# Kernel tuning notes

Measured on AMD Instinct MI355X. Metric: run time of the kernel, lower is better.

The kernel has to match this reference:

```python
import jax, jax.numpy as jnp
import numpy as np

N = 500_000
LEVELS = 3
GDIM = 8
BASE_H = 128
BASE_W = 128
COND = 64
DOUT = 128
HID = 2
DIN = 1 + 2 * LEVELS * GDIM  # rho + theta-grid feats + rho-grid feats = 49


def _bilinear(grid, u, v):
    # grid: [H, W, D]; u, v in [0,1]; u indexes W axis, v indexes H axis.
    H, W, D = grid.shape
    x = u * (W - 1)
    y = v * (H - 1)
    x0 = jnp.clip(jnp.floor(x).astype(jnp.int32), 0, W - 2)
    y0 = jnp.clip(jnp.floor(y).astype(jnp.int32), 0, H - 2)
    x1 = x0 + 1
    y1 = y0 + 1
    wx = (x - x0)[:, None]
    wy = (y - y0)[:, None]
    g = grid.reshape(H * W, D)
    c00 = jnp.take(g, y0 * W + x0, axis=0)
    c01 = jnp.take(g, y0 * W + x1, axis=0)
    c10 = jnp.take(g, y1 * W + x0, axis=0)
    c11 = jnp.take(g, y1 * W + x1, axis=0)
    return (c00 * (1 - wx) * (1 - wy) + c01 * wx * (1 - wy)
            + c10 * (1 - wx) * wy + c11 * wx * wy)


def setup_inputs() -> dict:
    key = jax.random.key(0)
    ks = jax.random.split(key, 24)
    inp = {
        'coords': jax.random.uniform(ks[0], (N,), dtype=jnp.float32),
        'angles': jax.random.uniform(ks[1], (N,), dtype=jnp.float32),
        'rho': jax.random.normal(ks[2], (N,), dtype=jnp.float32),
        'rho_n': jax.random.uniform(ks[3], (N,), dtype=jnp.float32),
        'curve_feats': jax.random.normal(ks[4], (N, COND), dtype=jnp.float32),
        'type_sample': jax.random.normal(ks[5], (N, DOUT), dtype=jnp.float32),
    }
    # Multi-resolution grids (theta-conditioned and rho-conditioned).
    for l in range(LEVELS):
        h, w = BASE_H * 2 ** l, BASE_W * 2 ** l
        inp[f'gt{l}'] = 0.1 * jax.random.normal(ks[6 + l], (h, w, GDIM), dtype=jnp.float32)
        inp[f'gr{l}'] = 0.1 * jax.random.normal(ks[9 + l], (h, w, GDIM), dtype=jnp.float32)
    # FiLM-modulated encoder chain (block 0 + HID residual blocks).
    inp['film0_fcW'] = jax.random.normal(ks[12], (DIN, DOUT), dtype=jnp.float32) / np.sqrt(DIN)
    inp['film0_fcb'] = jnp.zeros((DOUT,), dtype=jnp.float32)
    inp['filmh_fcW'] = jax.random.normal(ks[13], (HID, DOUT, DOUT), dtype=jnp.float32) / np.sqrt(DOUT)
    inp['filmh_fcb'] = jnp.zeros((HID, DOUT), dtype=jnp.float32)
    inp['gammaW'] = 0.02 * jax.random.normal(ks[14], (HID + 1, COND, DOUT), dtype=jnp.float32)
    inp['gammab'] = jnp.ones((HID + 1, DOUT), dtype=jnp.float32)
    inp['betaW'] = 0.02 * jax.random.normal(ks[15], (HID + 1, COND, DOUT), dtype=jnp.float32)
    inp['betab'] = jnp.zeros((HID + 1, DOUT), dtype=jnp.float32)
    # Decoder MLP [DOUT, 64, 1].
    inp['decW1'] = jax.random.normal(ks[16], (DOUT, 64), dtype=jnp.float32) / np.sqrt(DOUT)
    inp['decb1'] = jnp.zeros((64,), dtype=jnp.float32)
    inp['decW2'] = jax.random.normal(ks[17], (64, 1), dtype=jnp.float32) / 8.0
    inp['decb2'] = jnp.zeros((1,), dtype=jnp.float32)
    return inp


def reference(coords, angles, rho, rho_n, curve_feats, type_sample,
              gt0, gt1, gt2, gr0, gr1, gr2,
              film0_fcW, film0_fcb, filmh_fcW, filmh_fcb,
              gammaW, gammab, betaW, betab,
              decW1, decb1, decW2, decb2):
    # Multi-res grid interpolation, concat across levels.
    ct = jnp.concatenate([_bilinear(g, angles, coords) for g in (gt0, gt1, gt2)], axis=-1)
    cr = jnp.concatenate([_bilinear(g, rho_n, coords) for g in (gr0, gr1, gr2)], axis=-1)
    feat = jnp.concatenate([rho[:, None], ct, cr], axis=-1)  # [N, DIN]
    # FiLM conditioning: gamma/beta per block from curve_feats.
    gamma = jnp.einsum('nc,lcd->lnd', curve_feats, gammaW) + gammab[:, None, :]
    beta = jnp.einsum('nc,lcd->lnd', curve_feats, betaW) + betab[:, None, :]
    # Block 0 + type_sample residual.
    x = jax.nn.silu(gamma[0] * (feat @ film0_fcW + film0_fcb) + beta[0]) + type_sample
    # Residual FiLM blocks.
    for i in range(filmh_fcW.shape[0]):
        x = x + jax.nn.silu(gamma[i + 1] * (x @ filmh_fcW[i] + filmh_fcb[i]) + beta[i + 1])
    # Decoder MLP.
    h = jax.nn.relu(x @ decW1 + decb1)
    sdf = (h @ decW2 + decb2)[..., 0]  # [N]
    return sdf
```

## Files before the change

### kernel.cpp

```cpp
#include <hip/hip_runtime.h>
#include <stdint.h>

typedef short s16x8 __attribute__((ext_vector_type(8)));
typedef float f32x4 __attribute__((ext_vector_type(4)));
typedef uint32_t u32x4 __attribute__((ext_vector_type(4)));

#define MFMA16(a, b, c) __builtin_amdgcn_mfma_f32_16x16x32_bf16(a, b, c, 0, 0, 0)

__device__ __forceinline__ short f2bf(float f) {
  uint32_t u = __builtin_bit_cast(uint32_t, f);
  u += 0x7FFFu + ((u >> 16) & 1u);
  return (short)(u >> 16);
}
__device__ __forceinline__ uint32_t cvtpk(float lo, float hi) {
  uint32_t r;
  asm("v_cvt_pk_bf16_f32 %0, %1, %2" : "=v"(r) : "v"(lo), "v"(hi));
  return r;
}
__device__ __forceinline__ short f2bf1(float f) { return (short)cvtpk(f, f); }

__global__ void pack_w(const float* __restrict__ w0, const float* __restrict__ wh,
                       const float* __restrict__ gw, const float* __restrict__ bw,
                       const float* __restrict__ d1, const float* __restrict__ d1bp,
                       const float* __restrict__ d2wp, short* __restrict__ out,
                       float* __restrict__ dpk) {
  int idx = blockIdx.x * 512 + threadIdx.x;
  if (idx < 98304) {
    int f = idx >> 9;
    int r = idx & 511;
    int lane = r >> 3, e = r & 7;
    int kk = ((lane >> 4) << 3) + e;
    int nn = lane & 15;
    float v;
    if (f < 16) {
      int ct = f >> 1, ks = f & 1;
      int k = ks * 32 + kk, n = ct * 16 + nn;
      if (k < 48) v = w0[(1 + k) * 128 + n];
      else if (k == 48) v = w0[n];
      else v = 0.f;
    } else if (f < 112) {
      int f2 = f - 16;
      int ks = f2 & 1, ct = (f2 >> 1) & 7, gb = (f2 >> 4) & 1, l = f2 >> 5;
      int k = ks * 32 + kk, n = ct * 16 + nn;
      const float* Wp = gb ? bw : gw;
      v = Wp[(l * 64 + k) * 128 + n];
    } else if (f < 176) {
      int f2 = f - 112;
      int ks = f2 & 3, ct = (f2 >> 2) & 7, i = f2 >> 5;
      int k = ks * 32 + kk, n = ct * 16 + nn;
      v = wh[(i * 128 + k) * 128 + n];
    } else {
      int f2 = f - 176;
      int ks = f2 & 3, ct = f2 >> 2;
      int k = ks * 32 + kk, n = ct * 16 + nn;
      v = d1[k * 64 + n];
    }
    out[idx] = f2bf(v);
  } else if (idx < 100352) {
    int j = idx - 98304;
    int which = j >> 10;
    int k = j & 1023;
    int ct = k >> 8, lane = (k >> 2) & 63, rr = k & 3;
    int n2 = ct * 16 + ((lane >> 4) << 2) + rr;
    dpk[j] = which ? d2wp[n2] : d1bp[n2];
  }
}

__global__ __launch_bounds__(512) void ngc_gather(
    const float* __restrict__ coords, const float* __restrict__ angles,
    const float* __restrict__ rho, const float* __restrict__ rho_n,
    const float* __restrict__ gt0, const float* __restrict__ gr0,
    const float* __restrict__ gt1, const float* __restrict__ gr1,
    const float* __restrict__ gt2, const float* __restrict__ gr2,
    short* __restrict__ stage, int n, int t0) {
  const int tid = threadIdx.x;
  const int row0 = (t0 + blockIdx.x) * 64;
  char* st = (char*)(stage + (size_t)blockIdx.x * 4096);

  if (tid < 384) {
    int r = tid & 63, g = tid >> 6;
    int gr_ = row0 + r; gr_ = gr_ < n ? gr_ : n - 1;
    float vv = coords[gr_];
    float u = (g < 3) ? angles[gr_] : rho_n[gr_];
    int lvl = (g < 3) ? g : g - 3;
    const float* G = (g == 0) ? gt0 : (g == 1) ? gt1 : (g == 2) ? gt2
                   : (g == 3) ? gr0 : (g == 4) ? gr1 : gr2;
    int Wg = 128 << lvl;
    float x = u * (float)(Wg - 1), y = vv * (float)(Wg - 1);
    int ix = (int)x; ix = ix < 0 ? 0 : (ix > Wg - 2 ? Wg - 2 : ix);
    int iy = (int)y; iy = iy < 0 ? 0 : (iy > Wg - 2 ? Wg - 2 : iy);
    float wx = x - (float)ix, wy = y - (float)iy;
    const float4* p0 = (const float4*)(G + (size_t)(iy * Wg + ix) * 8);
    const float4* p1 = (const float4*)(G + (size_t)((iy + 1) * Wg + ix) * 8);
    float4 c00a = p0[0], c00b = p0[1], c01a = p0[2], c01b = p0[3];
    float4 c10a = p1[0], c10b = p1[1], c11a = p1[2], c11b = p1[3];
    float w00 = (1.f - wx) * (1.f - wy), w01 = wx * (1.f - wy);
    float w10 = (1.f - wx) * wy, w11 = wx * wy;
    float e0 = c00a.x * w00 + c01a.x * w01 + c10a.x * w10 + c11a.x * w11;
    float e1 = c00a.y * w00 + c01a.y * w01 + c10a.y * w10 + c11a.y * w11;
    float e2 = c00a.z * w00 + c01a.z * w01 + c10a.z * w10 + c11a.z * w11;
    float e3 = c00a.w * w00 + c01a.w * w01 + c10a.w * w10 + c11a.w * w11;
    float e4 = c00b.x * w00 + c01b.x * w01 + c10b.x * w10 + c11b.x * w11;
    float e5 = c00b.y * w00 + c01b.y * w01 + c10b.y * w10 + c11b.y * w11;
    float e6 = c00b.z * w00 + c01b.z * w01 + c10b.z * w10 + c11b.z * w11;
    float e7 = c00b.w * w00 + c01b.w * w01 + c10b.w * w10 + c11b.w * w11;
    u32x4 o = { cvtpk(e0, e1), cvtpk(e2, e3), cvtpk(e4, e5), cvtpk(e6, e7) };
    int dst16 = ((r >> 4) * 2 + (g >> 2)) * 64 + (g & 3) * 16 + (r & 15);
    *(u32x4*)(st + dst16 * 16) = o;
  } else if (tid < 448) {
    int r = tid - 384;
    int gr_ = row0 + r; gr_ = gr_ < n ? gr_ : n - 1;
    s16x8 a = { f2bf1(rho[gr_]), 0, 0, 0, 0, 0, 0, 0 };
    int base = ((r >> 4) * 2 + 1) * 64;
    *(s16x8*)(st + (base + 32 + (r & 15)) * 16) = a;
  } else {
    int r = tid - 448;
    s16x8 z = { 0, 0, 0, 0, 0, 0, 0, 0 };
    int base = ((r >> 4) * 2 + 1) * 64;
    *(s16x8*)(st + (base + 48 + (r & 15)) * 16) = z;
  }
}

__global__ __launch_bounds__(512) void ngc_gemm(
    const float* __restrict__ cf, const float* __restrict__ ts,
    const float* __restrict__ f0b, const float* __restrict__ fhb,
    const float* __restrict__ gab, const float* __restrict__ beb,
    const float* __restrict__ d2b, const short* __restrict__ pw,
    const float* __restrict__ dpk, const short* __restrict__ stage,
    float* __restrict__ out, int n, int t0) {
  __shared__ __align__(16) char smem[40 * 1024];
  char* cfA = smem;
  char* x0  = smem + 8 * 1024;
  char* x1  = smem + 24 * 1024;

  const int tid = threadIdx.x;
  const int lane = tid & 63;
  const int w = tid >> 6;
  const int g16 = lane >> 4;
  const int l15 = lane & 15;
  const int row0 = (t0 + blockIdx.x) * 64;
  const int col = w * 16 + l15;
  const int cbase = col >> 5;
  const int cslot = ((col >> 3) & 3) * 16;
  const int ce = (col & 7) * 2;

  const float d2b0 = d2b[0];

  float tsr[4][4];
#pragma unroll
  for (int rg = 0; rg < 4; ++rg)
#pragma unroll
    for (int rr = 0; rr < 4; ++rr) {
      int grow = row0 + rg * 16 + g16 * 4 + rr; grow = grow < n ? grow : n - 1;
      tsr[rg][rr] = ts[(size_t)grow * 128 + col];
    }

  {
    int cb = tid & 7, r = tid >> 3;
    int gr_ = row0 + r; gr_ = gr_ < n ? gr_ : n - 1;
    const float4* cp = (const float4*)(cf + (size_t)gr_ * 64 + cb * 8);
    float4 v0 = cp[0], v1 = cp[1];
    u32x4 s = { cvtpk(v0.x, v0.y), cvtpk(v0.z, v0.w),
                cvtpk(v1.x, v1.y), cvtpk(v1.z, v1.w) };
    int dst16 = ((r >> 4) * 2 + (cb >> 2)) * 64 + (cb & 3) * 16 + (r & 15);
    *(u32x4*)(cfA + dst16 * 16) = s;
  }
  __syncthreads();

  const s16x8* fB = (const s16x8*)stage + (size_t)blockIdx.x * 512;
  auto ldfeat = [&](int frag) -> s16x8 { return fB[frag * 64 + lane]; };
  auto ldF = [&](const char* b, int frag) -> s16x8 {
    return *(const s16x8*)(b + (frag * 64 + lane) * 16);
  };
  auto ldw = [&](int frag) -> s16x8 { return ((const s16x8*)pw)[frag * 64 + lane]; };

  float xr[4][4];

  {
    s16x8 bw0 = ldw(w * 2), bw1 = ldw(w * 2 + 1);
    s16x8 bg0 = ldw(16 + w * 2), bg1 = ldw(16 + w * 2 + 1);
    s16x8 bb0 = ldw(32 + w * 2), bb1 = ldw(32 + w * 2 + 1);
    float f0bv = f0b[col], gabv = gab[col], bebv = beb[col];
#pragma unroll
    for (int rg = 0; rg < 4; ++rg) {
      s16x8 a0 = ldfeat(rg * 2), a1 = ldfeat(rg * 2 + 1);
      s16x8 c0 = ldF(cfA, rg * 2), c1 = ldF(cfA, rg * 2 + 1);
      f32x4 t = {0.f, 0.f, 0.f, 0.f};
      t = MFMA16(a0, bw0, t); t = MFMA16(a1, bw1, t);
      f32x4 ga = {0.f, 0.f, 0.f, 0.f};
      ga = MFMA16(c0, bg0, ga); ga = MFMA16(c1, bg1, ga);
      f32x4 be = {0.f, 0.f, 0.f, 0.f};
      be = MFMA16(c0, bb0, be); be = MFMA16(c1, bb1, be);
      char* xbase = x0 + (rg * 4 + cbase) * 1024 + ce;
#pragma unroll
      for (int rr = 0; rr < 4; ++rr) {
        float z = (ga[rr] + gabv) * (t[rr] + f0bv) + (be[rr] + bebv);
        float sl = z * __builtin_amdgcn_rcpf(1.f + __expf(-z));
        xr[rg][rr] = sl + tsr[rg][rr];
        *(short*)(xbase + (cslot + g16 * 4 + rr) * 16) = f2bf1(xr[rg][rr]);
      }
    }
  }
  __syncthreads();

#pragma unroll
  for (int i = 0; i < 2; ++i) {
    const char* xsrc = i ? x1 : x0;
    char* xdst = i ? x0 : x1;
    s16x8 bh0 = ldw(112 + i * 32 + w * 4);
    s16x8 bh1 = ldw(112 + i * 32 + w * 4 + 1);
    s16x8 bh2 = ldw(112 + i * 32 + w * 4 + 2);
    s16x8 bh3 = ldw(112 + i * 32 + w * 4 + 3);
    s16x8 bg0 = ldw(16 + (i + 1) * 32 + w * 2);
    s16x8 bg1 = ldw(16 + (i + 1) * 32 + w * 2 + 1);
    s16x8 bb0 = ldw(16 + (i + 1) * 32 + 16 + w * 2);
    s16x8 bb1 = ldw(16 + (i + 1) * 32 + 16 + w * 2 + 1);
    float fhbv = fhb[i * 128 + col];
    float gabv = gab[(i + 1) * 128 + col];
    float bebv = beb[(i + 1) * 128 + col];
#pragma unroll
    for (int rg = 0; rg < 4; ++rg) {
      s16x8 xa = ldF(xsrc, rg * 4), xb = ldF(xsrc, rg * 4 + 1);
      s16x8 xc = ldF(xsrc, rg * 4 + 2), xd = ldF(xsrc, rg * 4 + 3);
      s16x8 c0 = ldF(cfA, rg * 2), c1 = ldF(cfA, rg * 2 + 1);
      f32x4 t = {0.f, 0.f, 0.f, 0.f};
      t = MFMA16(xa, bh0, t); t = MFMA16(xb, bh1, t);
      t = MFMA16(xc, bh2, t); t = MFMA16(xd, bh3, t);
      f32x4 ga = {0.f, 0.f, 0.f, 0.f};
      ga = MFMA16(c0, bg0, ga); ga = MFMA16(c1, bg1, ga);
      f32x4 be = {0.f, 0.f, 0.f, 0.f};
      be = MFMA16(c0, bb0, be); be = MFMA16(c1, bb1, be);
      char* xbase = xdst + (rg * 4 + cbase) * 1024 + ce;
#pragma unroll
      for (int rr = 0; rr < 4; ++rr) {
        float zz = (ga[rr] + gabv) * (t[rr] + fhbv) + (be[rr] + bebv);
        xr[rg][rr] += zz * __builtin_amdgcn_rcpf(1.f + __expf(-zz));
        *(short*)(xbase + (cslot + g16 * 4 + rr) * 16) = f2bf1(xr[rg][rr]);
      }
    }
    __syncthreads();
  }

  if (w < 4) {
    const int rg = w;
    s16x8 xF0 = ldF(x0, rg * 4), xF1 = ldF(x0, rg * 4 + 1);
    s16x8 xF2 = ldF(x0, rg * 4 + 2), xF3 = ldF(x0, rg * 4 + 3);
    float s = 0.f;
#pragma unroll
    for (int ct = 0; ct < 4; ++ct) {
      f32x4 hh = {0.f, 0.f, 0.f, 0.f};
      hh = MFMA16(ldw(176 + ct * 4 + 0), xF0, hh);
      hh = MFMA16(ldw(176 + ct * 4 + 1), xF1, hh);
      hh = MFMA16(ldw(176 + ct * 4 + 2), xF2, hh);
      hh = MFMA16(ldw(176 + ct * 4 + 3), xF3, hh);
      f32x4 db = *(const f32x4*)&dpk[ct * 256 + lane * 4];
      f32x4 wv = *(const f32x4*)&dpk[1024 + ct * 256 + lane * 4];
#pragma unroll
      for (int rr = 0; rr < 4; ++rr)
        s += fmaxf(hh[rr] + db[rr], 0.f) * wv[rr];
    }
    s += __shfl_xor(s, 16);
    s += __shfl_xor(s, 32);
    if (g16 == 0) {
      int grow = row0 + rg * 16 + l15;
      if (grow < n) out[grow] = s + d2b0;
    }
  }
}

extern "C" void kernel_launch(void* const* d_in, const int* in_sizes, int n_in,
                              void* d_out, int out_size, void* d_ws, size_t ws_size,
                              hipStream_t stream) {
  int n = in_sizes[0];
  short* pw = (short*)d_ws;
  float* dpk = (float*)((char*)d_ws + 192 * 1024);
  const size_t stage_off = 256 * 1024;
  short* stage = (short*)((char*)d_ws + stage_off);
  int ntiles = (n + 63) / 64;
  long long avail = (long long)ws_size - (long long)stage_off;
  int chunk = (int)(avail > 8192 ? avail / 8192 : 1);
  if (chunk > ntiles) chunk = ntiles;
  if (chunk < 1) chunk = 1;

  pack_w<<<196, 512, 0, stream>>>(
      (const float*)d_in[12],
      (const float*)d_in[14],
      (const float*)d_in[16],
      (const float*)d_in[18],
      (const float*)d_in[20],
      (const float*)d_in[21],
      (const float*)d_in[22],
      pw, dpk);

  for (int t0 = 0; t0 < ntiles; t0 += chunk) {
    int nb = ntiles - t0 < chunk ? ntiles - t0 : chunk;
    ngc_gather<<<nb, 512, 0, stream>>>(
        (const float*)d_in[0],
        (const float*)d_in[1],
        (const float*)d_in[2],
        (const float*)d_in[3],
        (const float*)d_in[6],
        (const float*)d_in[7],
        (const float*)d_in[8],
        (const float*)d_in[9],
        (const float*)d_in[10],
        (const float*)d_in[11],
        stage, n, t0);
    ngc_gemm<<<nb, 512, 0, stream>>>(
        (const float*)d_in[4],
        (const float*)d_in[5],
        (const float*)d_in[13],
        (const float*)d_in[15],
        (const float*)d_in[17],
        (const float*)d_in[19],
        (const float*)d_in[23],
        pw, dpk, stage, (float*)d_out, n, t0);
  }
}
```

Baseline: 271.5 us.

## Make GEMM kernel persistent with software-prefetch of next tile's inputs

The GEMM kernel becomes a grid-stride persistent loop capped at 1024 blocks. Each block prefetches the next tile's curve features and type_sample rows into registers while it computes the current tile. __syncthreads is replaced with a barrier that waits only on LDS (lgkmcnt), so the outstanding global prefetches are not drained at each barrier. This aims to hide global load latency and cut block launch overhead, at the cost of extra register pressure.

```diff
diff --git a/kernel.cpp b/kernel.cpp
--- a/kernel.cpp
+++ b/kernel.cpp
@@ -6,6 +6,7 @@
 typedef uint32_t u32x4 __attribute__((ext_vector_type(4)));
 
 #define MFMA16(a, b, c) __builtin_amdgcn_mfma_f32_16x16x32_bf16(a, b, c, 0, 0, 0)
+#define GEMM_BLK 1024
 
 __device__ __forceinline__ short f2bf(float f) {
   uint32_t u = __builtin_bit_cast(uint32_t, f);
@@ -18,6 +19,12 @@
   return r;
 }
 __device__ __forceinline__ short f2bf1(float f) { return (short)cvtpk(f, f); }
+
+__device__ __forceinline__ void bsync() {
+  asm volatile("s_waitcnt lgkmcnt(0)" ::: "memory");
+  __builtin_amdgcn_s_barrier();
+  asm volatile("" ::: "memory");
+}
 
 __global__ void pack_w(const float* __restrict__ w0, const float* __restrict__ wh,
                        const float* __restrict__ gw, const float* __restrict__ bw,
@@ -127,7 +134,7 @@
     const float* __restrict__ gab, const float* __restrict__ beb,
     const float* __restrict__ d2b, const short* __restrict__ pw,
     const float* __restrict__ dpk, const short* __restrict__ stage,
-    float* __restrict__ out, int n, int t0) {
+    float* __restrict__ out, int n, int t0, int ntc) {
   __shared__ __align__(16) char smem[40 * 1024];
   char* cfA = smem;
   char* x0  = smem + 8 * 1024;
@@ -138,132 +145,147 @@
   const int w = tid >> 6;
   const int g16 = lane >> 4;
   const int l15 = lane & 15;
-  const int row0 = (t0 + blockIdx.x) * 64;
   const int col = w * 16 + l15;
   const int cbase = col >> 5;
   const int cslot = ((col >> 3) & 3) * 16;
   const int ce = (col & 7) * 2;
+  const int cb = tid & 7, rcf = tid >> 3;
 
   const float d2b0 = d2b[0];
 
+  float4 cfr0, cfr1;
   float tsr[4][4];
-#pragma unroll
-  for (int rg = 0; rg < 4; ++rg)
-#pragma unroll
-    for (int rr = 0; rr < 4; ++rr) {
-      int grow = row0 + rg * 16 + g16 * 4 + rr; grow = grow < n ? grow : n - 1;
-      tsr[rg][rr] = ts[(size_t)grow * 128 + col];
-    }
-
-  {
-    int cb = tid & 7, r = tid >> 3;
-    int gr_ = row0 + r; gr_ = gr_ < n ? gr_ : n - 1;
+
+  auto issueA = [&](int tt2) {
+    int gr_ = (t0 + tt2) * 64 + rcf; gr_ = gr_ < n ? gr_ : n - 1;
     const float4* cp = (const float4*)(cf + (size_t)gr_ * 64 + cb * 8);
-    float4 v0 = cp[0], v1 = cp[1];
-    u32x4 s = { cvtpk(v0.x, v0.y), cvtpk(v0.z, v0.w),
-                cvtpk(v1.x, v1.y), cvtpk(v1.z, v1.w) };
-    int dst16 = ((r >> 4) * 2 + (cb >> 2)) * 64 + (cb & 3) * 16 + (r & 15);
-    *(u32x4*)(cfA + dst16 * 16) = s;
-  }
-  __syncthreads();
-
-  const s16x8* fB = (const s16x8*)stage + (size_t)blockIdx.x * 512;
-  auto ldfeat = [&](int frag) -> s16x8 { return fB[frag * 64 + lane]; };
+    cfr0 = cp[0]; cfr1 = cp[1];
+  };
+  auto issueT = [&](int tt2) {
+    int row0n = (t0 + tt2) * 64;
+#pragma unroll
+    for (int rg = 0; rg < 4; ++rg)
+#pragma unroll
+      for (int rr = 0; rr < 4; ++rr) {
+        int grow = row0n + rg * 16 + g16 * 4 + rr; grow = grow < n ? grow : n - 1;
+        tsr[rg][rr] = ts[(size_t)grow * 128 + col];
+      }
+  };
+
   auto ldF = [&](const char* b, int frag) -> s16x8 {
     return *(const s16x8*)(b + (frag * 64 + lane) * 16);
   };
   auto ldw = [&](int frag) -> s16x8 { return ((const s16x8*)pw)[frag * 64 + lane]; };
 
-  float xr[4][4];
-
-  {
-    s16x8 bw0 = ldw(w * 2), bw1 = ldw(w * 2 + 1);
-    s16x8 bg0 = ldw(16 + w * 2), bg1 = ldw(16 + w * 2 + 1);
-    s16x8 bb0 = ldw(32 + w * 2), bb1 = ldw(32 + w * 2 + 1);
-    float f0bv = f0b[col], gabv = gab[col], bebv = beb[col];
-#pragma unroll
-    for (int rg = 0; rg < 4; ++rg) {
-      s16x8 a0 = ldfeat(rg * 2), a1 = ldfeat(rg * 2 + 1);
-      s16x8 c0 = ldF(cfA, rg * 2), c1 = ldF(cfA, rg * 2 + 1);
-      f32x4 t = {0.f, 0.f, 0.f, 0.f};
-      t = MFMA16(a0, bw0, t); t = MFMA16(a1, bw1, t);
-      f32x4 ga = {0.f, 0.f, 0.f, 0.f};
-      ga = MFMA16(c0, bg0, ga); ga = MFMA16(c1, bg1, ga);
-      f32x4 be = {0.f, 0.f, 0.f, 0.f};
-      be = MFMA16(c0, bb0, be); be = MFMA16(c1, bb1, be);
-      char* xbase = x0 + (rg * 4 + cbase) * 1024 + ce;
-#pragma unroll
-      for (int rr = 0; rr < 4; ++rr) {
-        float z = (ga[rr] + gabv) * (t[rr] + f0bv) + (be[rr] + bebv);
-        float sl = z * __builtin_amdgcn_rcpf(1.f + __expf(-z));
-        xr[rg][rr] = sl + tsr[rg][rr];
-        *(short*)(xbase + (cslot + g16 * 4 + rr) * 16) = f2bf1(xr[rg][rr]);
-      }
-    }
-  }
-  __syncthreads();
-
-#pragma unroll
-  for (int i = 0; i < 2; ++i) {
-    const char* xsrc = i ? x1 : x0;
-    char* xdst = i ? x0 : x1;
-    s16x8 bh0 = ldw(112 + i * 32 + w * 4);
-    s16x8 bh1 = ldw(112 + i * 32 + w * 4 + 1);
-    s16x8 bh2 = ldw(112 + i * 32 + w * 4 + 2);
-    s16x8 bh3 = ldw(112 + i * 32 + w * 4 + 3);
-    s16x8 bg0 = ldw(16 + (i + 1) * 32 + w * 2);
-    s16x8 bg1 = ldw(16 + (i + 1) * 32 + w * 2 + 1);
-    s16x8 bb0 = ldw(16 + (i + 1) * 32 + 16 + w * 2);
-    s16x8 bb1 = ldw(16 + (i + 1) * 32 + 16 + w * 2 + 1);
-    float fhbv = fhb[i * 128 + col];
-    float gabv = gab[(i + 1) * 128 + col];
-    float bebv = beb[(i + 1) * 128 + col];
-#pragma unroll
-    for (int rg = 0; rg < 4; ++rg) {
-      s16x8 xa = ldF(xsrc, rg * 4), xb = ldF(xsrc, rg * 4 + 1);
-      s16x8 xc = ldF(xsrc, rg * 4 + 2), xd = ldF(xsrc, rg * 4 + 3);
-      s16x8 c0 = ldF(cfA, rg * 2), c1 = ldF(cfA, rg * 2 + 1);
-      f32x4 t = {0.f, 0.f, 0.f, 0.f};
-      t = MFMA16(xa, bh0, t); t = MFMA16(xb, bh1, t);
-      t = MFMA16(xc, bh2, t); t = MFMA16(xd, bh3, t);
-      f32x4 ga = {0.f, 0.f, 0.f, 0.f};
-      ga = MFMA16(c0, bg0, ga); ga = MFMA16(c1, bg1, ga);
-      f32x4 be = {0.f, 0.f, 0.f, 0.f};
-      be = MFMA16(c0, bb0, be); be = MFMA16(c1, bb1, be);
-      char* xbase = xdst + (rg * 4 + cbase) * 1024 + ce;
-#pragma unroll
-      for (int rr = 0; rr < 4; ++rr) {
-        float zz = (ga[rr] + gabv) * (t[rr] + fhbv) + (be[rr] + bebv);
-        xr[rg][rr] += zz * __builtin_amdgcn_rcpf(1.f + __expf(-zz));
-        *(short*)(xbase + (cslot + g16 * 4 + rr) * 16) = f2bf1(xr[rg][rr]);
-      }
-    }
-    __syncthreads();
-  }
-
-  if (w < 4) {
-    const int rg = w;
-    s16x8 xF0 = ldF(x0, rg * 4), xF1 = ldF(x0, rg * 4 + 1);
-    s16x8 xF2 = ldF(x0, rg * 4 + 2), xF3 = ldF(x0, rg * 4 + 3);
-    float s = 0.f;
-#pragma unroll
-    for (int ct = 0; ct < 4; ++ct) {
-      f32x4 hh = {0.f, 0.f, 0.f, 0.f};
-      hh = MFMA16(ldw(176 + ct * 4 + 0), xF0, hh);
-      hh = MFMA16(ldw(176 + ct * 4 + 1), xF1, hh);
-      hh = MFMA16(ldw(176 + ct * 4 + 2), xF2, hh);
-      hh = MFMA16(ldw(176 + ct * 4 + 3), xF3, hh);
-      f32x4 db = *(const f32x4*)&dpk[ct * 256 + lane * 4];
-      f32x4 wv = *(const f32x4*)&dpk[1024 + ct * 256 + lane * 4];
-#pragma unroll
-      for (int rr = 0; rr < 4; ++rr)
-        s += fmaxf(hh[rr] + db[rr], 0.f) * wv[rr];
-    }
-    s += __shfl_xor(s, 16);
-    s += __shfl_xor(s, 32);
-    if (g16 == 0) {
-      int grow = row0 + rg * 16 + l15;
-      if (grow < n) out[grow] = s + d2b0;
+  int tt = blockIdx.x;
+  if (tt < ntc) { issueA(tt); issueT(tt); }
+
+  for (; tt < ntc; tt += gridDim.x) {
+    const int row0 = (t0 + tt) * 64;
+    const int tn = tt + gridDim.x;
+    const s16x8* fB = (const s16x8*)stage + (size_t)tt * 512;
+
+    {
+      u32x4 s = { cvtpk(cfr0.x, cfr0.y), cvtpk(cfr0.z, cfr0.w),
+                  cvtpk(cfr1.x, cfr1.y), cvtpk(cfr1.z, cfr1.w) };
+      int dst16 = ((rcf >> 4) * 2 + (cb >> 2)) * 64 + (cb & 3) * 16 + (rcf & 15);
+      *(u32x4*)(cfA + dst16 * 16) = s;
+    }
+    if (tn < ntc) issueA(tn);
+    bsync();
+
+    float xr[4][4];
+
+    {
+      s16x8 bw0 = ldw(w * 2), bw1 = ldw(w * 2 + 1);
+      s16x8 bg0 = ldw(16 + w * 2), bg1 = ldw(16 + w * 2 + 1);
+      s16x8 bb0 = ldw(32 + w * 2), bb1 = ldw(32 + w * 2 + 1);
+      float f0bv = f0b[col], gabv = gab[col], bebv = beb[col];
+#pragma unroll
+      for (int rg = 0; rg < 4; ++rg) {
+        s16x8 a0 = fB[(rg * 2) * 64 + lane], a1 = fB[(rg * 2 + 1) * 64 + lane];
+        s16x8 c0 = ldF(cfA, rg * 2), c1 = ldF(cfA, rg * 2 + 1);
+        f32x4 t = {0.f, 0.f, 0.f, 0.f};
+        t = MFMA16(a0, bw0, t); t = MFMA16(a1, bw1, t);
+        f32x4 ga = {0.f, 0.f, 0.f, 0.f};
+        ga = MFMA16(c0, bg0, ga); ga = MFMA16(c1, bg1, ga);
+        f32x4 be = {0.f, 0.f, 0.f, 0.f};
+        be = MFMA16(c0, bb0, be); be = MFMA16(c1, bb1, be);
+        char* xbase = x0 + (rg * 4 + cbase) * 1024 + ce;
+#pragma unroll
+        for (int rr = 0; rr < 4; ++rr) {
+          float z = (ga[rr] + gabv) * (t[rr] + f0bv) + (be[rr] + bebv);
+          float sl = z * __builtin_amdgcn_rcpf(1.f + __expf(-z));
+          xr[rg][rr] = sl + tsr[rg][rr];
+          *(short*)(xbase + (cslot + g16 * 4 + rr) * 16) = f2bf1(xr[rg][rr]);
+        }
+      }
+    }
+    if (tn < ntc) issueT(tn);
+    bsync();
+
+#pragma unroll
+    for (int i = 0; i < 2; ++i) {
+      const char* xsrc = i ? x1 : x0;
+      char* xdst = i ? x0 : x1;
+      s16x8 bh0 = ldw(112 + i * 32 + w * 4);
+      s16x8 bh1 = ldw(112 + i * 32 + w * 4 + 1);
+      s16x8 bh2 = ldw(112 + i * 32 + w * 4 + 2);
+      s16x8 bh3 = ldw(112 + i * 32 + w * 4 + 3);
+      s16x8 bg0 = ldw(16 + (i + 1) * 32 + w * 2);
+      s16x8 bg1 = ldw(16 + (i + 1) * 32 + w * 2 + 1);
+      s16x8 bb0 = ldw(16 + (i + 1) * 32 + 16 + w * 2);
+      s16x8 bb1 = ldw(16 + (i + 1) * 32 + 16 + w * 2 + 1);
+      float fhbv = fhb[i * 128 + col];
+      float gabv = gab[(i + 1) * 128 + col];
+      float bebv = beb[(i + 1) * 128 + col];
+#pragma unroll
+      for (int rg = 0; rg < 4; ++rg) {
+        s16x8 xa = ldF(xsrc, rg * 4), xb = ldF(xsrc, rg * 4 + 1);
+        s16x8 xc = ldF(xsrc, rg * 4 + 2), xd = ldF(xsrc, rg * 4 + 3);
+        s16x8 c0 = ldF(cfA, rg * 2), c1 = ldF(cfA, rg * 2 + 1);
+        f32x4 t = {0.f, 0.f, 0.f, 0.f};
+        t = MFMA16(xa, bh0, t); t = MFMA16(xb, bh1, t);
+        t = MFMA16(xc, bh2, t); t = MFMA16(xd, bh3, t);
+        f32x4 ga = {0.f, 0.f, 0.f, 0.f};
+        ga = MFMA16(c0, bg0, ga); ga = MFMA16(c1, bg1, ga);
+        f32x4 be = {0.f, 0.f, 0.f, 0.f};
+        be = MFMA16(c0, bb0, be); be = MFMA16(c1, bb1, be);
+        char* xbase = xdst + (rg * 4 + cbase) * 1024 + ce;
+#pragma unroll
+        for (int rr = 0; rr < 4; ++rr) {
+          float zz = (ga[rr] + gabv) * (t[rr] + fhbv) + (be[rr] + bebv);
+          xr[rg][rr] += zz * __builtin_amdgcn_rcpf(1.f + __expf(-zz));
+          *(short*)(xbase + (cslot + g16 * 4 + rr) * 16) = f2bf1(xr[rg][rr]);
+        }
+      }
+      bsync();
+    }
+
+    if (w < 4) {
+      const int rg = w;
+      s16x8 xF0 = ldF(x0, rg * 4), xF1 = ldF(x0, rg * 4 + 1);
+      s16x8 xF2 = ldF(x0, rg * 4 + 2), xF3 = ldF(x0, rg * 4 + 3);
+      float s = 0.f;
+#pragma unroll
+      for (int ct = 0; ct < 4; ++ct) {
+        f32x4 hh = {0.f, 0.f, 0.f, 0.f};
+        hh = MFMA16(ldw(176 + ct * 4 + 0), xF0, hh);
+        hh = MFMA16(ldw(176 + ct * 4 + 1), xF1, hh);
+        hh = MFMA16(ldw(176 + ct * 4 + 2), xF2, hh);
+        hh = MFMA16(ldw(176 + ct * 4 + 3), xF3, hh);
+        f32x4 db = *(const f32x4*)&dpk[ct * 256 + lane * 4];
+        f32x4 wv = *(const f32x4*)&dpk[1024 + ct * 256 + lane * 4];
+#pragma unroll
+        for (int rr = 0; rr < 4; ++rr)
+          s += fmaxf(hh[rr] + db[rr], 0.f) * wv[rr];
+      }
+      s += __shfl_xor(s, 16);
+      s += __shfl_xor(s, 32);
+      if (g16 == 0) {
+        int grow = row0 + rg * 16 + l15;
+        if (grow < n) out[grow] = s + d2b0;
+      }
     }
   }
 }
@@ -306,7 +328,8 @@
         (const float*)d_in[10],
         (const float*)d_in[11],
         stage, n, t0);
-    ngc_gemm<<<nb, 512, 0, stream>>>(
+    int gb = nb < GEMM_BLK ? nb : GEMM_BLK;
+    ngc_gemm<<<gb, 512, 0, stream>>>(
         (const float*)d_in[4],
         (const float*)d_in[5],
         (const float*)d_in[13],
@@ -314,6 +337,6 @@
         (const float*)d_in[17],
         (const float*)d_in[19],
         (const float*)d_in[23],
-        pw, dpk, stage, (float*)d_out, n, t0);
+        pw, dpk, stage, (float*)d_out, n, t0, nb);
   }
 }
```

After: 333.8 us. 23.0% more time.
